# Kernel optimization log

Measured on AMD Instinct MI355X. Metric: run time of the kernel, lower is better.

## Reference

```python
import jax, jax.numpy as jnp
import numpy as np

B, N, K = 8, 2048, 16
C_IN, C_MID, C_OUT = 64, 16, 64
WH = [32, 32]
FH = [256]


def _mlp_params(key, dims, scale_keyed=True):
    ps = []
    for i in range(len(dims) - 1):
        key, k1 = jax.random.split(key)
        w = jax.random.normal(k1, (dims[i], dims[i + 1]), jnp.float32) / np.sqrt(dims[i])
        b = jnp.zeros((dims[i + 1],), jnp.float32)
        ps += [w, b]
    return ps


def setup_inputs() -> dict:
    key = jax.random.key(0)
    k1, k2, k3, k4, k5 = jax.random.split(key, 5)
    groups = jnp.broadcast_to(jnp.arange(N, dtype=jnp.int32) // K, (B, N))
    points = jax.random.normal(k1, (B, N, 3), jnp.float32)
    feats = jax.random.normal(k2, (B, N, C_IN), jnp.float32)
    point_mask = (jax.random.uniform(k3, (B, N)) > 0.1).astype(jnp.float32)
    w1, b1, w2, b2, w3, b3 = _mlp_params(k4, [3] + WH + [C_MID])
    f1, fb1, f2, fb2 = _mlp_params(k5, [C_IN * C_MID] + FH + [C_OUT])
    return {"groups": groups, "points": points, "feats": feats,
            "point_mask": point_mask,
            "w1": w1, "b1": b1, "w2": w2, "b2": b2, "w3": w3, "b3": b3,
            "f1": f1, "fb1": fb1, "f2": f2, "fb2": fb2}


def _neighbor_idxs(groups):
    # matches[b,i,j] = groups[b,i]==groups[b,j]; torch .nonzero yields, per (b,i),
    # the matching j in increasing order -> stable argsort of ~matches, take first K.
    matches = groups[:, :, None] == groups[:, None, :]            # [B,N,N]
    return jnp.argsort((~matches).astype(jnp.int32), axis=-1)[:, :, :K]  # [B,N,K]


def reference(groups, points, feats, point_mask,
              w1, b1, w2, b2, w3, b3, f1, fb1, f2, fb2):
    idxs = _neighbor_idxs(groups)                                  # [B,N,K] int
    gather = jax.vmap(lambda arr, ix: arr[ix])                     # per-batch gather
    nb_pts = gather(points, idxs)                                  # [B,N,K,3]
    nb_feats = gather(feats, idxs)                                 # [B,N,K,C_IN]
    rel = points[:, :, None, :] - nb_pts                           # [B,N,K,3] (xy encoding = identity)

    # weight_conv: pointwise MLP 3 -> 32 -> 32 -> C_MID, then explicit ReLU
    h = jax.nn.relu(rel @ w1 + b1)
    h = jax.nn.relu(h @ w2 + b2)
    m = jax.nn.relu(h @ w3 + b3)                                   # [B,N,K,C_MID]

    tmask = gather(point_mask, idxs)                               # [B,N,K]
    m = m * tmask[..., None]
    nb_feats = nb_feats * tmask[..., None]

    # per-(point) matmul: [C_MID,K] x [K,C_IN] -> flatten C_MID-major
    e = jnp.einsum('bnkm,bnkc->bnmc', m, nb_feats)                 # [B,N,C_MID,C_IN]
    e = e.reshape(B, N, C_MID * C_IN)

    # final_conv: pointwise MLP 1024 -> 256 -> C_OUT
    h2 = jax.nn.relu(e @ f1 + fb1)
    out = h2 @ f2 + fb2                                            # [B,N,C_OUT]
    return out
```

## Files before the change

### kernel.cpp

```cpp
#include <hip/hip_runtime.h>

typedef unsigned short u16;
typedef short bf16x8 __attribute__((ext_vector_type(8)));
typedef float f32x4  __attribute__((ext_vector_type(4)));
typedef u16   u16x4  __attribute__((ext_vector_type(4)));

__device__ __forceinline__ u16 f2bf(float f) {
  union { float f; unsigned int i; } v; v.f = f;
  unsigned int r = (v.i + 0x7FFFu + ((v.i >> 16) & 1u)) >> 16;
  return (u16)r;
}

__global__ __launch_bounds__(256) void repack_k(const float* __restrict__ f1,
                                                const float* __restrict__ f2,
                                                u16* __restrict__ f1p,
                                                u16* __restrict__ f2p) {
  const int o = blockIdx.x * 256 + threadIdx.x;
  if (o < 262144) {
    const int j = o & 7, n = (o >> 3) & 255, kb = o >> 11;
    f1p[o] = f2bf(f1[(kb * 8 + j) * 256 + n]);
  }
  if (o < 16384) {
    const int j = o & 7, n = (o >> 3) & 63, kb = o >> 9;
    f2p[o] = f2bf(f2[(kb * 8 + j) * 64 + n]);
  }
}

__global__ __launch_bounds__(256) void fused_k(
    const float* __restrict__ points, const float* __restrict__ feats,
    const float* __restrict__ pmask,
    const float* __restrict__ w1, const float* __restrict__ b1,
    const float* __restrict__ w2, const float* __restrict__ b2,
    const float* __restrict__ w3, const float* __restrict__ b3,
    const u16* __restrict__ f1p, const float* __restrict__ fb1,
    const u16* __restrict__ f2p, const float* __restrict__ fb2,
    float* __restrict__ out) {
  const int gi = blockIdx.x;
  const int bb = blockIdx.y;
  const int base = gi * 16;
  const int t = threadIdx.x;

  __shared__ float Wl[1712];
  __shared__ float Pl[16][3];
  __shared__ float Mask[16];
  __shared__ float F[1024];
  __shared__ __align__(16) u16 E[16 * 1032];
  __shared__ __align__(16) union {
    float Ml[16 * 16 * 17];
    u16   H2[16 * 264];
  } U;

  for (int idx = t; idx < 96;   idx += 256) Wl[idx]        = w1[idx];
  for (int idx = t; idx < 32;   idx += 256) Wl[96 + idx]   = b1[idx];
  for (int idx = t; idx < 1024; idx += 256) Wl[128 + idx]  = w2[idx];
  for (int idx = t; idx < 32;   idx += 256) Wl[1152 + idx] = b2[idx];
  for (int idx = t; idx < 512;  idx += 256) Wl[1184 + idx] = w3[idx];
  for (int idx = t; idx < 16;   idx += 256) Wl[1696 + idx] = b3[idx];
  if (t < 16) {
    Mask[t] = pmask[bb * 2048 + base + t];
    const int p = (bb * 2048 + base + t) * 3;
    Pl[t][0] = points[p + 0];
    Pl[t][1] = points[p + 1];
    Pl[t][2] = points[p + 2];
  }
  __syncthreads();

  for (int e = t; e < 1024; e += 256) {
    const int k = e >> 6;
    F[e] = feats[(bb * 2048 + base) * 64 + e] * Mask[k];
  }
  {
    const int i = t >> 4, k = t & 15;
    const float r0 = Pl[i][0] - Pl[k][0];
    const float r1 = Pl[i][1] - Pl[k][1];
    const float r2 = Pl[i][2] - Pl[k][2];
    float h1[32];
#pragma unroll
    for (int o = 0; o < 32; ++o) {
      float a = Wl[96 + o];
      a = fmaf(r0, Wl[o], a);
      a = fmaf(r1, Wl[32 + o], a);
      a = fmaf(r2, Wl[64 + o], a);
      h1[o] = fmaxf(a, 0.f);
    }
    float h2[32];
#pragma unroll
    for (int o = 0; o < 32; ++o) h2[o] = Wl[1152 + o];
#pragma unroll
    for (int j = 0; j < 32; ++j) {
      const float hj = h1[j];
      const float* w = &Wl[128 + j * 32];
#pragma unroll
      for (int o = 0; o < 32; ++o) h2[o] = fmaf(hj, w[o], h2[o]);
    }
#pragma unroll
    for (int o = 0; o < 32; ++o) h2[o] = fmaxf(h2[o], 0.f);
    float mo[16];
#pragma unroll
    for (int o = 0; o < 16; ++o) mo[o] = Wl[1696 + o];
#pragma unroll
    for (int j = 0; j < 32; ++j) {
      const float hj = h2[j];
      const float* w = &Wl[1184 + j * 16];
#pragma unroll
      for (int o = 0; o < 16; ++o) mo[o] = fmaf(hj, w[o], mo[o]);
    }
    const float mk = Mask[k];
    float* Mrow = &U.Ml[(i * 16 + k) * 17];
#pragma unroll
    for (int o = 0; o < 16; ++o) Mrow[o] = fmaxf(mo[o], 0.f) * mk;
  }
  __syncthreads();

  {
    const int i = t >> 4;
    const int c0 = (t & 15) * 4;
    float acc[16][4] = {};
#pragma unroll
    for (int k = 0; k < 16; ++k) {
      const float* Fr = &F[k * 64 + c0];
      const float f0 = Fr[0], fA = Fr[1], fB = Fr[2], fC = Fr[3];
      const float* Mrow = &U.Ml[(i * 16 + k) * 17];
#pragma unroll
      for (int mi = 0; mi < 16; ++mi) {
        const float mv = Mrow[mi];
        acc[mi][0] = fmaf(mv, f0, acc[mi][0]);
        acc[mi][1] = fmaf(mv, fA, acc[mi][1]);
        acc[mi][2] = fmaf(mv, fB, acc[mi][2]);
        acc[mi][3] = fmaf(mv, fC, acc[mi][3]);
      }
    }
    __syncthreads();
#pragma unroll
    for (int mi = 0; mi < 16; ++mi) {
      u16x4 v = { f2bf(acc[mi][0]), f2bf(acc[mi][1]), f2bf(acc[mi][2]), f2bf(acc[mi][3]) };
      *(u16x4*)&E[i * 1032 + mi * 64 + c0] = v;
    }
  }
  __syncthreads();

  {
    const int wv = t >> 6;
    const int lane = t & 63;
    const int q = lane >> 4, r16 = lane & 15;
    const int nb = wv * 64;
    f32x4 acc[4] = {};
    for (int ks = 0; ks < 32; ++ks) {
      const int k0 = ks * 32;
      const bf16x8 a = *(const bf16x8*)&E[r16 * 1032 + k0 + q * 8];
      const int kb = (k0 >> 3) + q;
#pragma unroll
      for (int nt = 0; nt < 4; ++nt) {
        const bf16x8 bv = *(const bf16x8*)&f1p[(kb * 256 + nb + nt * 16 + r16) * 8];
        acc[nt] = __builtin_amdgcn_mfma_f32_16x16x32_bf16(a, bv, acc[nt], 0, 0, 0);
      }
    }
    __syncthreads();
#pragma unroll
    for (int nt = 0; nt < 4; ++nt) {
      const int col = nb + nt * 16 + r16;
      const float bias = fb1[col];
#pragma unroll
      for (int r = 0; r < 4; ++r)
        U.H2[(q * 4 + r) * 264 + col] = f2bf(fmaxf(acc[nt][r] + bias, 0.f));
    }
  }
  __syncthreads();

  {
    const int wv = t >> 6;
    const int lane = t & 63;
    const int q = lane >> 4, r16 = lane & 15;
    const int n0 = wv * 16;
    f32x4 acc = {};
#pragma unroll
    for (int ks = 0; ks < 8; ++ks) {
      const int k0 = ks * 32;
      const bf16x8 a = *(const bf16x8*)&U.H2[r16 * 264 + k0 + q * 8];
      const bf16x8 bv = *(const bf16x8*)&f2p[(((k0 >> 3) + q) * 64 + n0 + r16) * 8];
      acc = __builtin_amdgcn_mfma_f32_16x16x32_bf16(a, bv, acc, 0, 0, 0);
    }
    const int col = n0 + r16;
    const float bias = fb2[col];
#pragma unroll
    for (int r = 0; r < 4; ++r) {
      const int row = q * 4 + r;
      out[((size_t)(bb * 2048 + base + row)) * 64 + col] = acc[r] + bias;
    }
  }
}

extern "C" void kernel_launch(void* const* d_in, const int* in_sizes, int n_in,
                              void* d_out, int out_size, void* d_ws, size_t ws_size,
                              hipStream_t stream) {
  const float* points = (const float*)d_in[1];
  const float* feats  = (const float*)d_in[2];
  const float* pmask  = (const float*)d_in[3];
  const float* w1 = (const float*)d_in[4];
  const float* b1 = (const float*)d_in[5];
  const float* w2 = (const float*)d_in[6];
  const float* b2 = (const float*)d_in[7];
  const float* w3 = (const float*)d_in[8];
  const float* b3 = (const float*)d_in[9];
  const float* f1 = (const float*)d_in[10];
  const float* fb1 = (const float*)d_in[11];
  const float* f2 = (const float*)d_in[12];
  const float* fb2 = (const float*)d_in[13];
  float* out = (float*)d_out;

  u16* f1p = (u16*)d_ws;
  u16* f2p = f1p + 262144;

  repack_k<<<dim3(1024), dim3(256), 0, stream>>>(f1, f2, f1p, f2p);
  fused_k<<<dim3(128, 8), dim3(256), 0, stream>>>(points, feats, pmask,
                                                  w1, b1, w2, b2, w3, b3,
                                                  f1p, fb1, f2p, fb2, out);
}
```

Before: 133.2 us.

## Split fused kernel into MLP stage and tiled double-buffered GEMM stage

Splits the single fused kernel into two. The first computes the weight MLP and the per-point contraction, then writes the bf16 E matrix to global workspace. The second runs the 1024->256->64 MLP over 64-row tiles with 512 threads, staging f1 tiles into LDS through double-buffered global_load_lds and prefetching the next A fragment. The aim is to cut the redundant f1 reads, since each 16-row block previously streamed all of f1 from global/L2. The cost is an extra global round trip for E (16 MB bf16), an extra launch, and fewer blocks in the GEMM stage.

```diff
diff --git a/kernel.cpp b/kernel.cpp
--- a/kernel.cpp
+++ b/kernel.cpp
@@ -9,6 +9,12 @@
   union { float f; unsigned int i; } v; v.f = f;
   unsigned int r = (v.i + 0x7FFFu + ((v.i >> 16) & 1u)) >> 16;
   return (u16)r;
+}
+
+__device__ __forceinline__ void gl16(const u16* g, u16* l) {
+  __builtin_amdgcn_global_load_lds(
+      (const __attribute__((address_space(1))) unsigned int*)g,
+      (__attribute__((address_space(3))) unsigned int*)l, 16, 0, 0);
 }
 
 __global__ __launch_bounds__(256) void repack_k(const float* __restrict__ f1,
@@ -26,15 +32,13 @@
   }
 }
 
-__global__ __launch_bounds__(256) void fused_k(
+__global__ __launch_bounds__(256) void k1_mlp(
     const float* __restrict__ points, const float* __restrict__ feats,
     const float* __restrict__ pmask,
     const float* __restrict__ w1, const float* __restrict__ b1,
     const float* __restrict__ w2, const float* __restrict__ b2,
     const float* __restrict__ w3, const float* __restrict__ b3,
-    const u16* __restrict__ f1p, const float* __restrict__ fb1,
-    const u16* __restrict__ f2p, const float* __restrict__ fb2,
-    float* __restrict__ out) {
+    u16* __restrict__ E) {
   const int gi = blockIdx.x;
   const int bb = blockIdx.y;
   const int base = gi * 16;
@@ -44,11 +48,7 @@
   __shared__ float Pl[16][3];
   __shared__ float Mask[16];
   __shared__ float F[1024];
-  __shared__ __align__(16) u16 E[16 * 1032];
-  __shared__ __align__(16) union {
-    float Ml[16 * 16 * 17];
-    u16   H2[16 * 264];
-  } U;
+  __shared__ float Ml[16 * 16 * 17];
 
   for (int idx = t; idx < 96;   idx += 256) Wl[idx]        = w1[idx];
   for (int idx = t; idx < 32;   idx += 256) Wl[96 + idx]   = b1[idx];
@@ -106,7 +106,7 @@
       for (int o = 0; o < 16; ++o) mo[o] = fmaf(hj, w[o], mo[o]);
     }
     const float mk = Mask[k];
-    float* Mrow = &U.Ml[(i * 16 + k) * 17];
+    float* Mrow = &Ml[(i * 16 + k) * 17];
 #pragma unroll
     for (int o = 0; o < 16; ++o) Mrow[o] = fmaxf(mo[o], 0.f) * mk;
   }
@@ -120,7 +120,7 @@
     for (int k = 0; k < 16; ++k) {
       const float* Fr = &F[k * 64 + c0];
       const float f0 = Fr[0], fA = Fr[1], fB = Fr[2], fC = Fr[3];
-      const float* Mrow = &U.Ml[(i * 16 + k) * 17];
+      const float* Mrow = &Ml[(i * 16 + k) * 17];
 #pragma unroll
       for (int mi = 0; mi < 16; ++mi) {
         const float mv = Mrow[mi];
@@ -130,62 +130,100 @@
         acc[mi][3] = fmaf(mv, fC, acc[mi][3]);
       }
     }
-    __syncthreads();
+    u16* Erow = &E[((size_t)(bb * 2048 + base + i)) * 1024];
 #pragma unroll
     for (int mi = 0; mi < 16; ++mi) {
       u16x4 v = { f2bf(acc[mi][0]), f2bf(acc[mi][1]), f2bf(acc[mi][2]), f2bf(acc[mi][3]) };
-      *(u16x4*)&E[i * 1032 + mi * 64 + c0] = v;
-    }
-  }
-  __syncthreads();
-
-  {
-    const int wv = t >> 6;
-    const int lane = t & 63;
-    const int q = lane >> 4, r16 = lane & 15;
-    const int nb = wv * 64;
-    f32x4 acc[4] = {};
-    for (int ks = 0; ks < 32; ++ks) {
-      const int k0 = ks * 32;
-      const bf16x8 a = *(const bf16x8*)&E[r16 * 1032 + k0 + q * 8];
-      const int kb = (k0 >> 3) + q;
-#pragma unroll
-      for (int nt = 0; nt < 4; ++nt) {
-        const bf16x8 bv = *(const bf16x8*)&f1p[(kb * 256 + nb + nt * 16 + r16) * 8];
-        acc[nt] = __builtin_amdgcn_mfma_f32_16x16x32_bf16(a, bv, acc[nt], 0, 0, 0);
-      }
+      *(u16x4*)&Erow[mi * 64 + c0] = v;
+    }
+  }
+}
+
+#define H2S 260
+__global__ __launch_bounds__(512) void k2_gemm(
+    const u16* __restrict__ E, const u16* __restrict__ f1p,
+    const float* __restrict__ fb1, const u16* __restrict__ f2p,
+    const float* __restrict__ fb2, float* __restrict__ out) {
+  __shared__ union {
+    u16 B[2][8192];
+    u16 H2[64 * H2S];
+  } S;
+
+  const int t = threadIdx.x;
+  const int w = t >> 6, lane = t & 63;
+  const int wr = w & 3, wc = w >> 2;
+  const int q = lane >> 4, r16 = lane & 15;
+  const int blk = blockIdx.x;
+
+  const int row = blk * 64 + wr * 16 + r16;
+  const u16* Arow = E + (size_t)row * 1024;
+
+  {
+    const u16* g = f1p;
+#pragma unroll
+    for (int c = 0; c < 2; ++c) {
+      const int off = (w * 2 + c) * 512;
+      gl16(g + off + lane * 8, &S.B[0][off]);
+    }
+  }
+  __syncthreads();
+
+  f32x4 acc[8] = {};
+  bf16x8 a_cur = *(const bf16x8*)(Arow + q * 8);
+  int buf = 0;
+  for (int ks = 0; ks < 32; ++ks) {
+    bf16x8 a_next;
+    if (ks < 31) {
+      const u16* g = f1p + (ks + 1) * 8192;
+#pragma unroll
+      for (int c = 0; c < 2; ++c) {
+        const int off = (w * 2 + c) * 512;
+        gl16(g + off + lane * 8, &S.B[buf ^ 1][off]);
+      }
+      a_next = *(const bf16x8*)(Arow + (ks + 1) * 32 + q * 8);
+    }
+#pragma unroll
+    for (int nt = 0; nt < 8; ++nt) {
+      const int col = wc * 128 + nt * 16 + r16;
+      const bf16x8 bv = *(const bf16x8*)&S.B[buf][(q * 256 + col) * 8];
+      acc[nt] = __builtin_amdgcn_mfma_f32_16x16x32_bf16(a_cur, bv, acc[nt], 0, 0, 0);
     }
     __syncthreads();
-#pragma unroll
-    for (int nt = 0; nt < 4; ++nt) {
-      const int col = nb + nt * 16 + r16;
-      const float bias = fb1[col];
-#pragma unroll
-      for (int r = 0; r < 4; ++r)
-        U.H2[(q * 4 + r) * 264 + col] = f2bf(fmaxf(acc[nt][r] + bias, 0.f));
-    }
-  }
-  __syncthreads();
-
-  {
-    const int wv = t >> 6;
-    const int lane = t & 63;
-    const int q = lane >> 4, r16 = lane & 15;
-    const int n0 = wv * 16;
-    f32x4 acc = {};
+    a_cur = a_next;
+    buf ^= 1;
+  }
+
+#pragma unroll
+  for (int nt = 0; nt < 8; ++nt) {
+    const int col = wc * 128 + nt * 16 + r16;
+    const float bias = fb1[col];
+#pragma unroll
+    for (int r = 0; r < 4; ++r)
+      S.H2[(wr * 16 + q * 4 + r) * H2S + col] = f2bf(fmaxf(acc[nt][r] + bias, 0.f));
+  }
+  __syncthreads();
+
+  {
+    f32x4 acc2[2] = {};
 #pragma unroll
     for (int ks = 0; ks < 8; ++ks) {
-      const int k0 = ks * 32;
-      const bf16x8 a = *(const bf16x8*)&U.H2[r16 * 264 + k0 + q * 8];
-      const bf16x8 bv = *(const bf16x8*)&f2p[(((k0 >> 3) + q) * 64 + n0 + r16) * 8];
-      acc = __builtin_amdgcn_mfma_f32_16x16x32_bf16(a, bv, acc, 0, 0, 0);
-    }
-    const int col = n0 + r16;
-    const float bias = fb2[col];
-#pragma unroll
-    for (int r = 0; r < 4; ++r) {
-      const int row = q * 4 + r;
-      out[((size_t)(bb * 2048 + base + row)) * 64 + col] = acc[r] + bias;
+      const bf16x8 a = *(const bf16x8*)&S.H2[(wr * 16 + r16) * H2S + ks * 32 + q * 8];
+#pragma unroll
+      for (int nt = 0; nt < 2; ++nt) {
+        const int col = wc * 32 + nt * 16 + r16;
+        const bf16x8 bv = *(const bf16x8*)&f2p[((ks * 4 + q) * 64 + col) * 8];
+        acc2[nt] = __builtin_amdgcn_mfma_f32_16x16x32_bf16(a, bv, acc2[nt], 0, 0, 0);
+      }
+    }
+#pragma unroll
+    for (int nt = 0; nt < 2; ++nt) {
+      const int col = wc * 32 + nt * 16 + r16;
+      const float bias = fb2[col];
+#pragma unroll
+      for (int r = 0; r < 4; ++r) {
+        const int rowg = blk * 64 + wr * 16 + q * 4 + r;
+        out[(size_t)rowg * 64 + col] = acc2[nt][r] + bias;
+      }
     }
   }
 }
@@ -210,9 +248,10 @@
 
   u16* f1p = (u16*)d_ws;
   u16* f2p = f1p + 262144;
+  u16* E   = f2p + 16384;
 
   repack_k<<<dim3(1024), dim3(256), 0, stream>>>(f1, f2, f1p, f2p);
-  fused_k<<<dim3(128, 8), dim3(256), 0, stream>>>(points, feats, pmask,
-                                                  w1, b1, w2, b2, w3, b3,
-                                                  f1p, fb1, f2p, fb2, out);
-}
+  k1_mlp<<<dim3(128, 8), dim3(256), 0, stream>>>(points, feats, pmask,
+                                                 w1, b1, w2, b2, w3, b3, E);
+  k2_gemm<<<dim3(256), dim3(512), 0, stream>>>(E, f1p, fb1, f2p, fb2, out);
+}
```

Result: slower. 148.2 us (+11.3%).
